# Performance work log

Hardware: AMD Instinct MI355X
Metric: run time of the kernel (lower is better)

Reference implementation:

```python
import jax, jax.numpy as jnp
import numpy as np

SEQ_LEN = 8192
D_K = 128
NEG_BIG = 1000000000.0


def setup_inputs() -> dict:
    key = jax.random.key(0)
    kq, kk, kv = jax.random.split(key, 3)
    q = jax.random.normal(kq, (SEQ_LEN, D_K), dtype=jnp.float32)
    k = jax.random.normal(kk, (SEQ_LEN, D_K), dtype=jnp.float32)
    v = jax.random.normal(kv, (SEQ_LEN, D_K), dtype=jnp.float32)
    return {"q": q, "k": k, "v": v}


def reference(q, k, v):
    # q,k,v: (S, d). Naive attention with causal (look-ahead) mask, masked=True.
    d_k = q.shape[-1]
    scaled_logits = jnp.matmul(q, k.T) / jnp.sqrt(jnp.asarray(d_k, q.dtype))  # (S, S)
    look_ahead_mask = jnp.triu(jnp.ones((SEQ_LEN, SEQ_LEN), dtype=q.dtype), k=1)
    scaled_logits = scaled_logits - look_ahead_mask * NEG_BIG
    attn = jnp.matmul(jax.nn.softmax(scaled_logits, axis=-1), v)  # (S, d)
    return attn
```

## Files before the change

kernel.cpp:

```cpp
#include <hip/hip_runtime.h>
#include <hip/hip_bf16.h>
#include <math.h>

#define S_LEN 8192
#define DK    128
#define BM    128
#define BN    64
#define NQT   (S_LEN / BM)
#define SCALE2 (0.08838834764831845f * 1.4426950408889634f)
#define DEFER_THR 5.0f

typedef __bf16 bf16x8_t __attribute__((ext_vector_type(8)));
typedef __bf16 bf16x4_t __attribute__((ext_vector_type(4)));
typedef __bf16 bf16x2_t __attribute__((ext_vector_type(2)));
typedef float  floatx16 __attribute__((ext_vector_type(16)));
typedef unsigned uintx4 __attribute__((ext_vector_type(4)));
typedef _Float16 half_t;
typedef _Float16 halfx4 __attribute__((ext_vector_type(4)));
typedef _Float16 halfx2 __attribute__((ext_vector_type(2)));

#define GLD16(g, l) __builtin_amdgcn_global_load_lds(                      \
    (const __attribute__((address_space(1))) void*)(g),                    \
    (__attribute__((address_space(3))) void*)(l), 16, 0, 0)

__device__ __forceinline__ float fexp2(float x) {
#if __has_builtin(__builtin_amdgcn_exp2f)
  return __builtin_amdgcn_exp2f(x);
#else
  return exp2f(x);
#endif
}

__device__ __forceinline__ unsigned pack2(float a, float b) {
  bf16x2_t w; w[0] = (__bf16)a; w[1] = (__bf16)b;
  return __builtin_bit_cast(unsigned, w);
}

__device__ __forceinline__ void xswap(unsigned &x, unsigned &y) {
#if __has_builtin(__builtin_amdgcn_permlane32_swap)
  typedef unsigned v2u __attribute__((ext_vector_type(2)));
  v2u t = __builtin_amdgcn_permlane32_swap(x, y, false, false);
  x = t[0]; y = t[1];
#else
  const unsigned sx = (unsigned)__shfl_xor((int)x, 32);
  const unsigned sy = (unsigned)__shfl_xor((int)y, 32);
  const bool lo = ((threadIdx.x & 63) < 32);
  const unsigned nx = lo ? x : sy;
  const unsigned ny = lo ? sx : y;
  x = nx; y = ny;
#endif
}

#define KBLOCKS ((S_LEN * DK) / (256 * 4))
__global__ __launch_bounds__(256) void prep_kv(const float* __restrict__ K,
                                               const float* __restrict__ V,
                                               __bf16* __restrict__ Kb,
                                               __bf16* __restrict__ Vt) {
  const int bx  = blockIdx.x;
  const int tid = threadIdx.x;
  if (bx < KBLOCKS) {
    const int i = (bx * 256 + tid) * 4;
    float4 v = *(const float4*)&K[i];
    bf16x4_t b;
    b[0] = (__bf16)v.x; b[1] = (__bf16)v.y; b[2] = (__bf16)v.z; b[3] = (__bf16)v.w;
    *(bf16x4_t*)&Kb[i] = b;
    return;
  }
  __shared__ __bf16 tl[64][34];
  const int vblk = bx - KBLOCKS;
  const int key0 = (vblk >> 2) * 64;
  const int d0   = (vblk & 3) * 32;
  {
    const int r = tid >> 2, fb = tid & 3;
    const float* vp = V + (size_t)(key0 + r) * DK + d0;
    #pragma unroll
    for (int h = 0; h < 2; ++h) {
      const int f = fb + h * 4;
      float4 v = *(const float4*)(vp + f * 4);
      tl[r][f * 4 + 0] = (__bf16)v.x; tl[r][f * 4 + 1] = (__bf16)v.y;
      tl[r][f * 4 + 2] = (__bf16)v.z; tl[r][f * 4 + 3] = (__bf16)v.w;
    }
  }
  __syncthreads();
  const int d = tid >> 3, kg = tid & 7;
  bf16x8_t b;
  #pragma unroll
  for (int j = 0; j < 8; ++j) b[j] = tl[kg * 8 + j][d];
  *(bf16x8_t*)&Vt[(size_t)(d0 + d) * S_LEN + key0 + kg * 8] = b;
}

__global__ __launch_bounds__(256, 3)
void fa_part(const float* __restrict__ Q, const __bf16* __restrict__ Kb,
             const __bf16* __restrict__ Vtg, float* __restrict__ Out,
             half_t* __restrict__ Opart, float* __restrict__ stats, int C) {
  __shared__ __align__(16) __bf16 Ks[2][BN * DK];
  __shared__ __align__(16) __bf16 Vts[DK * BN];

  const int tid  = threadIdx.x;
  const int wave = tid >> 6;
  const int lane = tid & 63;
  const int l31  = lane & 31;
  const int hh   = lane >> 5;

  const int qtile = (NQT - 1) - blockIdx.x;
  const int g     = blockIdx.y;
  const int nt    = 2 * qtile + 2;
  const int jb0   = g * C;
  if (jb0 >= nt) return;
  const int jb1 = (jb0 + C < nt) ? (jb0 + C) : nt;

  const int h2 = C >> 1;
  const int direct = (qtile < h2);
  const int ca = qtile / h2, cr = qtile - ca * h2;
  const int chunk = h2 * ca * (ca + 1) / 2 + cr * (ca + 1) - h2 + g;

  const int qw  = qtile * BM + wave * 32;
  const int myq = qw + l31;

  bf16x8_t qf[8];
  {
    const float* qrow = Q + (size_t)myq * DK + hh * 8;
    #pragma unroll
    for (int s = 0; s < 8; ++s) {
      float4 x = *(const float4*)(qrow + s * 16);
      float4 y = *(const float4*)(qrow + s * 16 + 4);
      bf16x8_t f;
      f[0]=(__bf16)(x.x*SCALE2); f[1]=(__bf16)(x.y*SCALE2);
      f[2]=(__bf16)(x.z*SCALE2); f[3]=(__bf16)(x.w*SCALE2);
      f[4]=(__bf16)(y.x*SCALE2); f[5]=(__bf16)(y.y*SCALE2);
      f[6]=(__bf16)(y.z*SCALE2); f[7]=(__bf16)(y.w*SCALE2);
      qf[s] = f;
    }
  }

  const __bf16* kp[4]; const __bf16* vp[4]; int loff[4];
  {
    const int ck = (lane & 15) ^ ((wave * 4 + (lane >> 4)) & 15);
    const int cv = (lane & 7) ^ ((lane >> 3) & 7);
    #pragma unroll
    for (int t = 0; t < 4; ++t) {
      const int rk = t * 16 + wave * 4 + (lane >> 4);
      kp[t] = Kb + ((size_t)(jb0 * BN + rk)) * DK + ck * 8;
      const int rv = t * 32 + wave * 8 + (lane >> 3);
      vp[t] = Vtg + (size_t)rv * S_LEN + jb0 * BN + cv * 8;
      loff[t] = t * 2048 + wave * 512;
    }
  }

  floatx16 o_acc[4];
  #pragma unroll
  for (int d = 0; d < 4; ++d)
    #pragma unroll
    for (int r = 0; r < 16; ++r) o_acc[d][r] = 0.f;
  float m_r = -INFINITY, l_r = 0.f;

  #pragma unroll
  for (int t = 0; t < 4; ++t) { GLD16(kp[t], &Ks[0][loff[t]]); kp[t] += BN * DK; }
  __syncthreads();

  int cur = 0;
  for (int jb = jb0; jb < jb1; ++jb) {
    #pragma unroll
    for (int t = 0; t < 4; ++t) { GLD16(vp[t], &Vts[loff[t]]); vp[t] += BN; }
    if (jb + 1 < jb1) {
      #pragma unroll
      for (int t = 0; t < 4; ++t) { GLD16(kp[t], &Ks[cur ^ 1][loff[t]]); kp[t] += BN * DK; }
    }

    const int active = (jb * 64 <= qw + 31);
    unsigned pk[4][4];

    if (active) {
      const __bf16* Kc = Ks[cur];

      floatx16 sv[2];
      __builtin_amdgcn_s_setprio(1);
      #pragma unroll
      for (int g1 = 0; g1 < 2; ++g1) {
        floatx16 acc;
        #pragma unroll
        for (int r = 0; r < 16; ++r) acc[r] = 0.f;
        const int row = g1 * 32 + l31;
        #pragma unroll
        for (int s = 0; s < 8; ++s) {
          bf16x8_t kf = *(const bf16x8_t*)
              &Kc[row * DK + (((s * 2 + hh) ^ (row & 15)) * 8)];
          acc = __builtin_amdgcn_mfma_f32_32x32x16_bf16(kf, qf[s], acc, 0, 0, 0);
        }
        sv[g1] = acc;
      }
      __builtin_amdgcn_s_setprio(0);

      if (jb * 64 + 63 > qw) {
        #pragma unroll
        for (int g1 = 0; g1 < 2; ++g1)
          #pragma unroll
          for (int r = 0; r < 16; ++r) {
            const int key = jb * 64 + g1 * 32 + (r & 3) + ((r >> 2) << 3) + (hh << 2);
            if (key > myq) sv[g1][r] = -1e30f;
          }
      }

      float pmx[4];
      #pragma unroll
      for (int i = 0; i < 4; ++i)
        pmx[i] = fmaxf(fmaxf(sv[0][i], sv[0][i + 4]),
                       fmaxf(sv[0][i + 8], sv[0][i + 12]));
      #pragma unroll
      for (int i = 0; i < 4; ++i)
        pmx[i] = fmaxf(pmx[i], fmaxf(fmaxf(sv[1][i], sv[1][i + 4]),
                                     fmaxf(sv[1][i + 8], sv[1][i + 12])));
      float pm = fmaxf(fmaxf(pmx[0], pmx[1]), fmaxf(pmx[2], pmx[3]));
      {
        unsigned b0 = __builtin_bit_cast(unsigned, pm), b1 = b0;
        xswap(b0, b1);
        pm = fmaxf(__builtin_bit_cast(float, b0), __builtin_bit_cast(float, b1));
      }

      if (__any(pm > m_r + DEFER_THR)) {
        const float mn = fmaxf(m_r, pm);
        const float al = fexp2(m_r - mn);
        m_r = mn; l_r *= al;
        #pragma unroll
        for (int d = 0; d < 4; ++d)
          #pragma unroll
          for (int r = 0; r < 16; ++r) o_acc[d][r] *= al;
      }

      float rsx[4] = {0.f, 0.f, 0.f, 0.f};
      #pragma unroll
      for (int g1 = 0; g1 < 2; ++g1)
        #pragma unroll
        for (int r = 0; r < 16; ++r) {
          const float pv = fexp2(sv[g1][r] - m_r);
          sv[g1][r] = pv;
          rsx[r & 3] += pv;
        }
      float rs = (rsx[0] + rsx[1]) + (rsx[2] + rsx[3]);
      {
        unsigned b0 = __builtin_bit_cast(unsigned, rs), b1 = b0;
        xswap(b0, b1);
        l_r += __builtin_bit_cast(float, b0) + __builtin_bit_cast(float, b1);
      }

      #pragma unroll
      for (int g1 = 0; g1 < 2; ++g1) {
        unsigned W0 = pack2(sv[g1][0],  sv[g1][1]);
        unsigned W1 = pack2(sv[g1][2],  sv[g1][3]);
        unsigned W2 = pack2(sv[g1][4],  sv[g1][5]);
        unsigned W3 = pack2(sv[g1][6],  sv[g1][7]);
        unsigned W4 = pack2(sv[g1][8],  sv[g1][9]);
        unsigned W5 = pack2(sv[g1][10], sv[g1][11]);
        unsigned W6 = pack2(sv[g1][12], sv[g1][13]);
        unsigned W7 = pack2(sv[g1][14], sv[g1][15]);
        xswap(W0, W2); xswap(W1, W3);
        xswap(W4, W6); xswap(W5, W7);
        pk[g1*2+0][0]=W0; pk[g1*2+0][1]=W1; pk[g1*2+0][2]=W2; pk[g1*2+0][3]=W3;
        pk[g1*2+1][0]=W4; pk[g1*2+1][1]=W5; pk[g1*2+1][2]=W6; pk[g1*2+1][3]=W7;
      }
    }

    __syncthreads();

    if (active) {
      __builtin_amdgcn_s_setprio(1);
      #pragma unroll
      for (int ks = 0; ks < 4; ++ks) {
        uintx4 u; u[0]=pk[ks][0]; u[1]=pk[ks][1]; u[2]=pk[ks][2]; u[3]=pk[ks][3];
        const bf16x8_t pf = __builtin_bit_cast(bf16x8_t, u);
        #pragma unroll
        for (int d = 0; d < 4; ++d) {
          const int row = d * 32 + l31;
          bf16x8_t vf = *(const bf16x8_t*)
              &Vts[row * BN + (((ks * 2 + hh) ^ (row & 7)) * 8)];
          o_acc[d] = __builtin_amdgcn_mfma_f32_32x32x16_bf16(vf, pf, o_acc[d], 0, 0, 0);
        }
      }
      __builtin_amdgcn_s_setprio(0);
    }

    __syncthreads();
    cur ^= 1;
  }

  if (direct) {
    const float inv = (l_r > 0.f) ? (1.0f / l_r) : 0.f;
    float* orow = Out + (size_t)myq * DK;
    #pragma unroll
    for (int d = 0; d < 4; ++d)
      #pragma unroll
      for (int mI = 0; mI < 4; ++mI) {
        float4 st;
        st.x = o_acc[d][mI*4+0] * inv; st.y = o_acc[d][mI*4+1] * inv;
        st.z = o_acc[d][mI*4+2] * inv; st.w = o_acc[d][mI*4+3] * inv;
        *(float4*)&orow[d * 32 + mI * 8 + hh * 4] = st;
      }
  } else {
    const float inv = (l_r > 0.f) ? (1.0f / l_r) : 0.f;
    half_t* orow = Opart + ((size_t)chunk * BM + wave * 32 + l31) * DK;
    #pragma unroll
    for (int d = 0; d < 4; ++d)
      #pragma unroll
      for (int mI = 0; mI < 4; ++mI) {
        halfx4 st;
        st[0] = (half_t)(o_acc[d][mI*4+0] * inv);
        st[1] = (half_t)(o_acc[d][mI*4+1] * inv);
        st[2] = (half_t)(o_acc[d][mI*4+2] * inv);
        st[3] = (half_t)(o_acc[d][mI*4+3] * inv);
        *(halfx4*)&orow[d * 32 + mI * 8 + hh * 4] = st;
      }
    if (hh == 0) {
      stats[((size_t)chunk * BM + wave * 32 + l31) * 2 + 0] = m_r;
      stats[((size_t)chunk * BM + wave * 32 + l31) * 2 + 1] = l_r;
    }
  }
}

__global__ __launch_bounds__(256)
void fa_reduce(const half_t* __restrict__ Opart, const float* __restrict__ stats,
               float* __restrict__ O, int C) {
  const int h2 = C >> 1;
  const int wave = threadIdx.x >> 6, lane = threadIdx.x & 63;
  const int row = h2 * BM + blockIdx.x * 4 + wave;
  const int qt = row >> 7, r = row & 127;

  const int a = qt / h2, rr = qt - a * h2;
  const int base = h2 * a * (a + 1) / 2 + rr * (a + 1) - h2;
  const int nch = (qt + h2) / h2;

  float M = -INFINITY;
  for (int g = 0; g < nch; ++g)
    M = fmaxf(M, stats[((size_t)(base + g) * BM + r) * 2]);

  float L = 0.f, ax = 0.f, ay = 0.f;
  for (int g = 0; g < nch; ++g) {
    const size_t sidx = (size_t)(base + g) * BM + r;
    const float m = stats[sidx * 2];
    const float wl = fexp2(m - M) * stats[sidx * 2 + 1];
    L += wl;
    halfx2 o = *(const halfx2*)&Opart[sidx * DK + lane * 2];
    ax += wl * (float)o[0]; ay += wl * (float)o[1];
  }
  const float inv = 1.f / L;
  float2 res; res.x = ax * inv; res.y = ay * inv;
  *(float2*)&O[(size_t)row * DK + lane * 2] = res;
}

extern "C" void kernel_launch(void* const* d_in, const int* in_sizes, int n_in,
                              void* d_out, int out_size, void* d_ws, size_t ws_size,
                              hipStream_t stream) {
  (void)in_sizes; (void)n_in; (void)out_size;
  const float* q = (const float*)d_in[0];
  const float* k = (const float*)d_in[1];
  const float* v = (const float*)d_in[2];
  float* out = (float*)d_out;

  const size_t conv_bytes = (size_t)S_LEN * DK * 2 * 2;
  const size_t per_chunk  = (size_t)BM * DK * 2 + 2 * BM * 4;
  const long long SLOTS   = 256 * 3;

  int C = 2 * NQT; long long nc = 0;
  for (int c = 4; c < 2 * NQT; c += 2) {
    const int hh2 = c / 2;
    const int a = NQT / hh2, rr = NQT - a * hh2;
    const long long F64 = (long long)hh2 * a * (a + 1) / 2 + (long long)rr * (a + 1);
    const long long n = F64 - hh2;
    const long long blocks = n + hh2;
    if (blocks <= SLOTS && conv_bytes + (size_t)n * per_chunk <= ws_size) {
      C = c; nc = n; break;
    }
  }

  __bf16* Kb = (__bf16*)d_ws;
  __bf16* Vt = Kb + (size_t)S_LEN * DK;
  half_t* Opart = (half_t*)(Vt + (size_t)S_LEN * DK);
  float* stats = (float*)(Opart + (size_t)nc * BM * DK);

  prep_kv<<<KBLOCKS + 512, 256, 0, stream>>>(k, v, Kb, Vt);

  const int gy = (2 * NQT + C - 1) / C;
  fa_part<<<dim3(NQT, gy), 256, 0, stream>>>(q, Kb, Vt, out, Opart, stats, C);

  if (nc > 0) {
    const int h2 = C / 2;
    const int nrows = (NQT - h2) * BM;
    fa_reduce<<<nrows / 4, 256, 0, stream>>>(Opart, stats, out, C);
  }
}
```

Measured before the change: 132.0 us.

## Double query tile to 256 rows with 8 waves per block sharing K/V tiles

Raises the query tile from 128 to 256 rows and launches 512-thread blocks, so eight waves share each staged K and V tile instead of four. Each thread now issues half as many async global-to-LDS loads per tile. The split-KV chunking, the chunk indexing and the reduce kernel are rederived for four key tiles per query tile. This is meant to halve K/V traffic per query row and the work of staging it. In exchange the grid has fewer, larger blocks, which may hurt load balance on the causal triangle, and the launch bound of 4 blocks per CU tightens register limits.

```diff
diff --git a/kernel.cpp b/kernel.cpp
--- a/kernel.cpp
+++ b/kernel.cpp
@@ -4,9 +4,9 @@
 
 #define S_LEN 8192
 #define DK    128
-#define BM    128
+#define BM    256
 #define BN    64
-#define NQT   (S_LEN / BM)
+#define NQT2  (S_LEN / BM)
 #define SCALE2 (0.08838834764831845f * 1.4426950408889634f)
 #define DEFER_THR 5.0f
 
@@ -89,7 +89,7 @@
   *(bf16x8_t*)&Vt[(size_t)(d0 + d) * S_LEN + key0 + kg * 8] = b;
 }
 
-__global__ __launch_bounds__(256, 3)
+__global__ __launch_bounds__(512, 4)
 void fa_part(const float* __restrict__ Q, const __bf16* __restrict__ Kb,
              const __bf16* __restrict__ Vtg, float* __restrict__ Out,
              half_t* __restrict__ Opart, float* __restrict__ stats, int C) {
@@ -102,17 +102,17 @@
   const int l31  = lane & 31;
   const int hh   = lane >> 5;
 
-  const int qtile = (NQT - 1) - blockIdx.x;
+  const int qtile = (NQT2 - 1) - blockIdx.x;
   const int g     = blockIdx.y;
-  const int nt    = 2 * qtile + 2;
+  const int nt    = 4 * qtile + 4;
   const int jb0   = g * C;
   if (jb0 >= nt) return;
   const int jb1 = (jb0 + C < nt) ? (jb0 + C) : nt;
 
-  const int h2 = C >> 1;
-  const int direct = (qtile < h2);
-  const int ca = qtile / h2, cr = qtile - ca * h2;
-  const int chunk = h2 * ca * (ca + 1) / 2 + cr * (ca + 1) - h2 + g;
+  const int h4 = C >> 2;
+  const int direct = (qtile < h4);
+  const int ca = qtile / h4, cr = qtile - ca * h4;
+  const int chunk = h4 * ca * (ca + 1) / 2 + cr * (ca + 1) - h4 + g;
 
   const int qw  = qtile * BM + wave * 32;
   const int myq = qw + l31;
@@ -133,17 +133,17 @@
     }
   }
 
-  const __bf16* kp[4]; const __bf16* vp[4]; int loff[4];
+  const __bf16* kp[2]; const __bf16* vp[2]; int lof[2];
   {
     const int ck = (lane & 15) ^ ((wave * 4 + (lane >> 4)) & 15);
     const int cv = (lane & 7) ^ ((lane >> 3) & 7);
     #pragma unroll
-    for (int t = 0; t < 4; ++t) {
-      const int rk = t * 16 + wave * 4 + (lane >> 4);
+    for (int t = 0; t < 2; ++t) {
+      const int rk = t * 32 + wave * 4 + (lane >> 4);
       kp[t] = Kb + ((size_t)(jb0 * BN + rk)) * DK + ck * 8;
-      const int rv = t * 32 + wave * 8 + (lane >> 3);
+      const int rv = t * 64 + wave * 8 + (lane >> 3);
       vp[t] = Vtg + (size_t)rv * S_LEN + jb0 * BN + cv * 8;
-      loff[t] = t * 2048 + wave * 512;
+      lof[t] = t * 4096 + wave * 512;
     }
   }
 
@@ -155,16 +155,16 @@
   float m_r = -INFINITY, l_r = 0.f;
 
   #pragma unroll
-  for (int t = 0; t < 4; ++t) { GLD16(kp[t], &Ks[0][loff[t]]); kp[t] += BN * DK; }
+  for (int t = 0; t < 2; ++t) { GLD16(kp[t], &Ks[0][lof[t]]); kp[t] += BN * DK; }
   __syncthreads();
 
   int cur = 0;
   for (int jb = jb0; jb < jb1; ++jb) {
     #pragma unroll
-    for (int t = 0; t < 4; ++t) { GLD16(vp[t], &Vts[loff[t]]); vp[t] += BN; }
+    for (int t = 0; t < 2; ++t) { GLD16(vp[t], &Vts[lof[t]]); vp[t] += BN; }
     if (jb + 1 < jb1) {
       #pragma unroll
-      for (int t = 0; t < 4; ++t) { GLD16(kp[t], &Ks[cur ^ 1][loff[t]]); kp[t] += BN * DK; }
+      for (int t = 0; t < 2; ++t) { GLD16(kp[t], &Ks[cur ^ 1][lof[t]]); kp[t] += BN * DK; }
     }
 
     const int active = (jb * 64 <= qw + 31);
@@ -319,14 +319,14 @@
 __global__ __launch_bounds__(256)
 void fa_reduce(const half_t* __restrict__ Opart, const float* __restrict__ stats,
                float* __restrict__ O, int C) {
-  const int h2 = C >> 1;
+  const int h4 = C >> 2;
   const int wave = threadIdx.x >> 6, lane = threadIdx.x & 63;
-  const int row = h2 * BM + blockIdx.x * 4 + wave;
-  const int qt = row >> 7, r = row & 127;
-
-  const int a = qt / h2, rr = qt - a * h2;
-  const int base = h2 * a * (a + 1) / 2 + rr * (a + 1) - h2;
-  const int nch = (qt + h2) / h2;
+  const int row = h4 * BM + blockIdx.x * 4 + wave;
+  const int qt = row >> 8, r = row & (BM - 1);
+
+  const int a = qt / h4, rr = qt - a * h4;
+  const int base = h4 * a * (a + 1) / 2 + rr * (a + 1) - h4;
+  const int nch = (qt + h4) / h4;
 
   float M = -INFINITY;
   for (int g = 0; g < nch; ++g)
@@ -359,13 +359,14 @@
   const size_t per_chunk  = (size_t)BM * DK * 2 + 2 * BM * 4;
   const long long SLOTS   = 256 * 3;
 
-  int C = 2 * NQT; long long nc = 0;
-  for (int c = 4; c < 2 * NQT; c += 2) {
-    const int hh2 = c / 2;
-    const int a = NQT / hh2, rr = NQT - a * hh2;
-    const long long F64 = (long long)hh2 * a * (a + 1) / 2 + (long long)rr * (a + 1);
-    const long long n = F64 - hh2;
-    const long long blocks = n + hh2;
+  int C = 4 * NQT2; long long nc = 0;
+  for (int c = 4; c < 4 * NQT2; c += 4) {
+    const int h4 = c / 4;
+    if (h4 >= NQT2) break;
+    const int a = NQT2 / h4, rr = NQT2 - a * h4;
+    const long long F64 = (long long)h4 * a * (a + 1) / 2 + (long long)rr * (a + 1);
+    const long long n = F64 - h4;
+    const long long blocks = n + h4;
     if (blocks <= SLOTS && conv_bytes + (size_t)n * per_chunk <= ws_size) {
       C = c; nc = n; break;
     }
@@ -378,12 +379,12 @@
 
   prep_kv<<<KBLOCKS + 512, 256, 0, stream>>>(k, v, Kb, Vt);
 
-  const int gy = (2 * NQT + C - 1) / C;
-  fa_part<<<dim3(NQT, gy), 256, 0, stream>>>(q, Kb, Vt, out, Opart, stats, C);
+  const int gy = (4 * NQT2 + C - 1) / C;
+  fa_part<<<dim3(NQT2, gy), 512, 0, stream>>>(q, Kb, Vt, out, Opart, stats, C);
 
   if (nc > 0) {
-    const int h2 = C / 2;
-    const int nrows = (NQT - h2) * BM;
+    const int h4 = C / 4;
+    const int nrows = (NQT2 - h4) * BM;
     fa_reduce<<<nrows / 4, 256, 0, stream>>>(Opart, stats, out, C);
   }
 }
```

New measurement: 222.9 us. 68.9% more time.
